# Performance work log

Hardware: AMD Instinct MI355X
Metric: run time of the kernel (lower is better)

## Reference

```python
import jax, jax.numpy as jnp
import numpy as np

N_NODES = 40000
N_EDGES = 640000
EMBED = 128
L = 3
EPS = 1e-5


def bn(x, g, b):
    # BatchNorm1d in training mode: batch mean / biased variance over axis 0
    m = jnp.mean(x, axis=0)
    v = jnp.var(x, axis=0)
    return (x - m) * jax.lax.rsqrt(v + EPS) * g + b


def setup_inputs() -> dict:
    key = jax.random.key(0)
    ks = jax.random.split(key, 16)
    d = {}
    d["node_attr"] = jax.random.normal(ks[0], (N_NODES, 2), jnp.float32)
    d["edge_index"] = jax.random.randint(ks[1], (2, N_EDGES), 0, N_NODES, jnp.int32)
    d["edge_attr"] = jax.random.normal(ks[2], (N_EDGES, 1), jnp.float32)
    s = 0.1
    d["W0"] = jax.random.normal(ks[3], (2, EMBED), jnp.float32) * s
    d["b0"] = jnp.zeros((EMBED,), jnp.float32)
    d["g0"] = jnp.ones((EMBED,), jnp.float32)
    d["bt0"] = jnp.zeros((EMBED,), jnp.float32)
    d["Wnode"] = jax.random.normal(ks[4], (L, EMBED, EMBED), jnp.float32) * s
    d["bnode"] = jnp.zeros((L, EMBED), jnp.float32)
    d["Wedge"] = jax.random.normal(ks[5], (L, 1, EMBED), jnp.float32) * s
    d["bedge"] = jnp.zeros((L, EMBED), jnp.float32)
    d["Wnb"] = jax.random.normal(ks[6], (L, EMBED, EMBED), jnp.float32) * s
    d["bnb"] = jnp.zeros((L, EMBED), jnp.float32)
    for nm in ("gn", "ge", "gnb", "gm1", "gm2"):
        d[nm] = jnp.ones((L, EMBED), jnp.float32)
    for nm in ("btn", "bte", "btnb", "btm1", "btm2"):
        d[nm] = jnp.zeros((L, EMBED), jnp.float32)
    d["Wm1"] = jax.random.normal(ks[7], (L, EMBED, EMBED), jnp.float32) * s
    d["bm1"] = jnp.zeros((L, EMBED), jnp.float32)
    d["Wm2"] = jax.random.normal(ks[8], (L, EMBED, EMBED), jnp.float32) * s
    d["bm2"] = jnp.zeros((L, EMBED), jnp.float32)
    return d


def reference(node_attr, edge_index, edge_attr,
              W0, b0, g0, bt0,
              Wnode, bnode, Wedge, bedge, Wnb, bnb,
              gn, btn, ge, bte, gnb, btnb,
              Wm1, bm1, gm1, btm1, Wm2, bm2, gm2, btm2):
    row, col = edge_index[0], edge_index[1]
    n = node_attr.shape[0]
    # initial node MLP (applied once, before layer 0)
    x = jax.nn.relu(bn(node_attr @ W0 + b0, g0, bt0))  # [N, E]
    for i in range(L):
        # edge branch: linear on raw edge_attr, scatter-add to source nodes (row)
        ea = edge_attr @ Wedge[i] + bedge[i]                      # [Ne, E]
        ea = jax.ops.segment_sum(ea, row, num_segments=n)         # [N, E]
        ea = bn(ea, ge[i], bte[i])
        # neighbor branch: h_j gathered from sources, aggregated at targets (col)
        h = x @ Wnb[i] + bnb[i]                                   # [N, E]
        aggr = jax.ops.segment_sum(h[row], col, num_segments=n)   # [N, E]
        # node branch
        xn = bn(x @ Wnode[i] + bnode[i], gn[i], btn[i])
        # update MLP
        y = jax.nn.relu(xn + bn(aggr, gnb[i], btnb[i]) + ea)
        y = jax.nn.relu(bn(y @ Wm1[i] + bm1[i], gm1[i], btm1[i]))
        y = jax.nn.relu(bn(y @ Wm2[i] + bm2[i], gm2[i], btm2[i]))
        x = y
    return x
```

## Files before the change

kernel.cpp:

```cpp
#include <hip/hip_runtime.h>

#define N_NODES 40000
#define N_EDGES 640000
#define EMB 128
#define NF ((size_t)N_NODES * EMB)
#define RCP_N (1.0f / (float)N_NODES)
#define BN_EPS 1e-5f
#define CAP 64
#define NSLICE 16
#define STB (NSLICE * 256)
#define GB 625

typedef _Float16 f16x8v __attribute__((ext_vector_type(8)));
typedef float f32x4v __attribute__((ext_vector_type(4)));
typedef unsigned short ushort8v __attribute__((ext_vector_type(8)));

__device__ __forceinline__ unsigned short f2h(float v) {
    return __builtin_bit_cast(unsigned short, (_Float16)v);
}
__device__ __forceinline__ float h2f(unsigned short u) {
    return (float)__builtin_bit_cast(_Float16, u);
}

__device__ __forceinline__ void bn_prep(
    const float* __restrict__ stat, const float* __restrict__ g,
    const float* __restrict__ bt, float* C, float* D, int t)
{
    if (t < 128) {
        float sm = 0.f, sq = 0.f;
        #pragma unroll
        for (int s = 0; s < NSLICE; ++s) {
            sm += stat[s * 256 + t];
            sq += stat[s * 256 + 128 + t];
        }
        float m = sm * RCP_N;
        float v = sq * RCP_N - m * m;
        float a = g[t] * rsqrtf(v + BN_EPS);
        C[t] = a; D[t] = bt[t] - m * a;
    }
}

__global__ __launch_bounds__(256) void edge_init_kernel(
    const float* __restrict__ na, const float* __restrict__ W0,
    const float* __restrict__ b0, unsigned short* __restrict__ Z,
    float* __restrict__ st,
    const int* __restrict__ ei, const float* __restrict__ ea,
    unsigned long long* __restrict__ scP, unsigned* __restrict__ cursor,
    int* __restrict__ slot)
{
    __shared__ float red[256];
    const int blk = blockIdx.x;
    const int t = threadIdx.x;
    if (blk < 625) {
        int col = t & 127, rh = t >> 7;
        float w0 = W0[col], w1 = W0[128 + col], bb = b0[col];
        int rbase = blk * 64;
        float sm = 0.f, sq = 0.f;
        #pragma unroll 4
        for (int i = 0; i < 32; ++i) {
            int r = rbase + rh + i * 2;
            float2 nv = *(const float2*)&na[r * 2];
            float v = fmaf(nv.x, w0, fmaf(nv.y, w1, bb));
            Z[(size_t)r * 128 + col] = f2h(v);
            sm += v; sq += v * v;
        }
        float* stS = st + (blk & (NSLICE - 1)) * 256;
        red[t] = sm; __syncthreads();
        if (t < 128) atomicAdd(&stS[t], red[t] + red[t + 128]);
        __syncthreads();
        red[t] = sq; __syncthreads();
        if (t < 128) atomicAdd(&stS[128 + t], red[t] + red[t + 128]);
    } else {
        int e = (blk - 625) * 256 + t;
        int r = ei[e];
        int d = ei[N_EDGES + e];
        int fx = (int)rintf(ea[e] * 65536.0f);
        unsigned long long add =
            (((unsigned long long)(unsigned)(fx + 0x40000000)) << 20) | 1ULL;
        atomicAdd(&scP[r], add);
        unsigned pos = atomicAdd(&cursor[d], 1u);
        slot[(size_t)d * CAP + (pos < CAP ? pos : CAP - 1)] = r;
    }
}

__global__ __launch_bounds__(256) void decode_kernel(
    const unsigned long long* __restrict__ scP, const unsigned* __restrict__ cursor,
    float* __restrict__ sN, float* __restrict__ cN, float* __restrict__ dgf,
    float* __restrict__ mom)
{
    int t = threadIdx.x;
    int i = blockIdx.x * 256 + t;
    float a0 = 0.f, a1 = 0.f, a2 = 0.f, a3 = 0.f, a4 = 0.f;
    if (i < N_NODES) {
        unsigned long long v = scP[i];
        unsigned cnt = (unsigned)(v & 0xFFFFFULL);
        long long sp = (long long)(v >> 20) - ((long long)cnt << 30);
        float s = (float)sp * (1.0f / 65536.0f);
        float c = (float)cnt;
        sN[i] = s; cN[i] = c;
        dgf[i] = (float)cursor[i];
        a0 = s; a1 = s * s; a2 = c; a3 = c * c; a4 = s * c;
    }
    #pragma unroll
    for (int off = 32; off > 0; off >>= 1) {
        a0 += __shfl_down(a0, off);
        a1 += __shfl_down(a1, off);
        a2 += __shfl_down(a2, off);
        a3 += __shfl_down(a3, off);
        a4 += __shfl_down(a4, off);
    }
    if ((t & 63) == 0) {
        atomicAdd(&mom[0], a0);
        atomicAdd(&mom[1], a1);
        atomicAdd(&mom[2], a2);
        atomicAdd(&mom[3], a3);
        atomicAdd(&mom[4], a4);
    }
}

__global__ __launch_bounds__(256) void wprep_kernel(
    const float* __restrict__ Wnode, const float* __restrict__ Wnb,
    const float* __restrict__ Wm1, const float* __restrict__ Wm2,
    unsigned short* __restrict__ Wt)
{
    __shared__ float tile[32][129];
    int b = blockIdx.x;
    int mat = b >> 2, kc = (b & 3) * 32;
    int grp = mat / 3, lay = mat % 3;
    const float* src = (grp == 0) ? Wnode : (grp == 1) ? Wnb : (grp == 2) ? Wm1 : Wm2;
    src += (size_t)lay * 16384;
    int t = threadIdx.x;
    #pragma unroll
    for (int i = 0; i < 16; ++i) {
        int idx = t + i * 256;
        int r = idx >> 7, n = idx & 127;
        tile[r][n] = src[(size_t)(kc + r) * 128 + n];
    }
    __syncthreads();
    int n = t >> 1, h = (t & 1) * 16;
    ushort8v o0, o1;
    #pragma unroll
    for (int j = 0; j < 8; ++j) o0[j] = f2h(tile[h + j][n]);
    #pragma unroll
    for (int j = 0; j < 8; ++j) o1[j] = f2h(tile[h + 8 + j][n]);
    unsigned short* dst = &Wt[(size_t)mat * 16384 + n * 128 + kc + h];
    *(ushort8v*)dst = o0;
    *(ushort8v*)(dst + 8) = o1;
}

__global__ __launch_bounds__(256) void gather_bn_kernel(
    const unsigned* __restrict__ cnt, const int* __restrict__ slot,
    const unsigned short* __restrict__ Ph,
    const float* __restrict__ stat, const float* __restrict__ g_in,
    const float* __restrict__ bt_in,
    unsigned short* __restrict__ Gh)
{
    __shared__ float aT[128], bT[128];
    int t = threadIdx.x;
    bn_prep(stat, g_in, bt_in, aT, bT, t);
    __syncthreads();
    int wid = (blockIdx.x * 256 + t) >> 6;
    int lane = t & 63;
    int q = lane >> 4, l16 = lane & 15;
    int cb = l16 * 8;
    float av[8], bv[8];
    #pragma unroll
    for (int k = 0; k < 8; ++k) { av[k] = aT[cb + k]; bv[k] = bT[cb + k]; }
    int n = (int)cnt[wid];
    n = n < CAP ? n : CAP;
    const int* sl = &slot[(size_t)wid * CAP];
    float s0[8] = {0}, s1[8] = {0};
    int j = q;
    for (; j + 4 < n; j += 8) {
        int r0 = sl[j], r1 = sl[j + 4];
        ushort8v v0 = *(const ushort8v*)&Ph[(size_t)r0 * 128 + cb];
        ushort8v v1 = *(const ushort8v*)&Ph[(size_t)r1 * 128 + cb];
        #pragma unroll
        for (int k = 0; k < 8; ++k) {
            s0[k] += fmaxf(0.f, fmaf(h2f(v0[k]), av[k], bv[k]));
            s1[k] += fmaxf(0.f, fmaf(h2f(v1[k]), av[k], bv[k]));
        }
    }
    for (; j < n; j += 4) {
        int r0 = sl[j];
        ushort8v v0 = *(const ushort8v*)&Ph[(size_t)r0 * 128 + cb];
        #pragma unroll
        for (int k = 0; k < 8; ++k)
            s0[k] += fmaxf(0.f, fmaf(h2f(v0[k]), av[k], bv[k]));
    }
    #pragma unroll
    for (int k = 0; k < 8; ++k) {
        float v = s0[k] + s1[k];
        v += __shfl_xor(v, 16);
        v += __shfl_xor(v, 32);
        s0[k] = v;
    }
    if (q == 0) {
        ushort8v o;
        #pragma unroll
        for (int k = 0; k < 8; ++k) o[k] = f2h(s0[k]);
        *(ushort8v*)&Gh[(size_t)wid * 128 + cb] = o;
    }
}

template<int AMODE, bool RSC>
__device__ __forceinline__ void gemm_body(
    int row0, int t, int slice,
    const unsigned short* __restrict__ A, const unsigned short* __restrict__ A2,
    const unsigned short* __restrict__ Wt,
    const float* __restrict__ bias, const float* __restrict__ rowscale,
    const float* C1, const float* D1, const float* C2, const float* D2,
    const float* AE, const float* BE, const float* CE,
    const float* __restrict__ sN, const float* __restrict__ cN,
    unsigned short* __restrict__ Out, float* __restrict__ stats_out,
    unsigned short* Bs, float (*redS)[128], float (*redQ)[128])
{
    #pragma unroll
    for (int i = 0; i < 8; ++i) {
        int cch = t + i * 256;
        int n = cch >> 4, off = (cch & 15) << 3;
        ushort8v w = *(const ushort8v*)&Wt[n * 128 + off];
        *(ushort8v*)&Bs[(n * 128 + off) ^ ((n & 7) << 3)] = w;
    }

    const int w = t >> 6, lane = t & 63;
    const int la = lane & 15, lb = lane >> 4;
    const int ar = row0 + (w << 4) + la;
    const int kb = lb * 8;

    f16x8v afrag[4];
    #pragma unroll
    for (int s = 0; s < 4; ++s) {
        ushort8v avv = *(const ushort8v*)&A[(size_t)ar * 128 + s * 32 + kb];
        if (AMODE == 0) {
            afrag[s] = __builtin_bit_cast(f16x8v, avv);
        } else if (AMODE == 1) {
            f16x8v o;
            #pragma unroll
            for (int j = 0; j < 8; ++j) {
                int qq = s * 32 + kb + j;
                o[j] = (_Float16)fmaxf(0.f, fmaf(h2f(avv[j]), C1[qq], D1[qq]));
            }
            afrag[s] = o;
        } else {
            ushort8v gv = *(const ushort8v*)&A2[(size_t)ar * 128 + s * 32 + kb];
            float sr = sN[ar], cr = cN[ar];
            f16x8v o;
            #pragma unroll
            for (int j = 0; j < 8; ++j) {
                int qq = s * 32 + kb + j;
                float y = h2f(avv[j]) * C1[qq] + D1[qq] + h2f(gv[j]) * C2[qq] + D2[qq]
                        + sr * AE[qq] + cr * BE[qq] + CE[qq];
                o[j] = (_Float16)fmaxf(0.f, y);
            }
            afrag[s] = o;
        }
    }
    __syncthreads();

    f32x4v acc[8];
    #pragma unroll
    for (int c = 0; c < 8; ++c) acc[c] = (f32x4v){0.f, 0.f, 0.f, 0.f};

    #pragma unroll
    for (int c = 0; c < 8; ++c) {
        int bn_ = (c << 4) + la;
        int bbase = bn_ * 128;
        int bswz = (bn_ & 7) << 3;
        #pragma unroll
        for (int s = 0; s < 4; ++s) {
            f16x8v bf = *(const f16x8v*)&Bs[(bbase + s * 32 + kb) ^ bswz];
            acc[c] = __builtin_amdgcn_mfma_f32_16x16x32_f16(
                afrag[s], bf, acc[c], 0, 0, 0);
        }
    }

    const int orow0 = row0 + (w << 4) + lb * 4;
    float rsj[4];
    if (RSC) {
        #pragma unroll
        for (int j = 0; j < 4; ++j) rsj[j] = rowscale[orow0 + j];
    }
    float csum[8], csq[8];
    #pragma unroll
    for (int c = 0; c < 8; ++c) {
        int col = (c << 4) + la;
        float bc = bias[col];
        float s0 = 0.f, s1 = 0.f;
        #pragma unroll
        for (int j = 0; j < 4; ++j) {
            float v = acc[c][j] + (RSC ? rsj[j] * bc : bc);
            Out[(size_t)(orow0 + j) * 128 + col] = f2h(v);
            s0 += v; s1 += v * v;
        }
        csum[c] = s0; csq[c] = s1;
    }
    #pragma unroll
    for (int c = 0; c < 8; ++c) {
        csum[c] += __shfl_xor(csum[c], 16);
        csum[c] += __shfl_xor(csum[c], 32);
        csq[c]  += __shfl_xor(csq[c], 16);
        csq[c]  += __shfl_xor(csq[c], 32);
    }
    if (lane < 16) {
        #pragma unroll
        for (int c = 0; c < 8; ++c) {
            redS[w][(c << 4) + lane] = csum[c];
            redQ[w][(c << 4) + lane] = csq[c];
        }
    }
    __syncthreads();
    float* stS = stats_out + slice * 256;
    if (t < 128) {
        atomicAdd(&stS[t], redS[0][t] + redS[1][t] + redS[2][t] + redS[3][t]);
        atomicAdd(&stS[128 + t], redQ[0][t] + redQ[1][t] + redQ[2][t] + redQ[3][t]);
    }
}

__global__ __launch_bounds__(256) void dual_gemm_kernel(
    const unsigned short* __restrict__ Ph, unsigned short* __restrict__ Gh,
    const unsigned short* __restrict__ WtZ, const unsigned short* __restrict__ WtG,
    const float* __restrict__ bZ, const float* __restrict__ bG,
    const float* __restrict__ dg,
    const float* __restrict__ st1, const float* __restrict__ g1,
    const float* __restrict__ bt1,
    unsigned short* __restrict__ ZNh,
    float* __restrict__ statZN, float* __restrict__ statG)
{
    __shared__ __align__(16) unsigned short Bs[128 * 128];
    __shared__ float C1[128], D1[128];
    __shared__ float redS[4][128], redQ[4][128];
    const int t = threadIdx.x;
    const int b = blockIdx.x;

    if (b < GB) {
        bn_prep(st1, g1, bt1, C1, D1, t);
        __syncthreads();
        gemm_body<1, false>(b * 64, t, b & (NSLICE - 1),
            Ph, nullptr, WtZ, bZ, nullptr,
            C1, D1, nullptr, nullptr, nullptr, nullptr, nullptr,
            nullptr, nullptr, ZNh, statZN, Bs, redS, redQ);
    } else {
        gemm_body<0, true>((b - GB) * 64, t, b & (NSLICE - 1),
            Gh, nullptr, WtG, bG, dg,
            nullptr, nullptr, nullptr, nullptr, nullptr, nullptr, nullptr,
            nullptr, nullptr, Gh, statG, Bs, redS, redQ);
    }
}

template<int AMODE, bool RSC>
__global__ __launch_bounds__(256) void mfma_gemm_kernel(
    const unsigned short* __restrict__ A, const unsigned short* __restrict__ A2,
    const unsigned short* __restrict__ Wt,
    const float* __restrict__ bias, const float* __restrict__ rowscale,
    const float* __restrict__ st1, const float* __restrict__ g1, const float* __restrict__ bt1,
    const float* __restrict__ st2, const float* __restrict__ g2, const float* __restrict__ bt2,
    const float* __restrict__ sN, const float* __restrict__ cN,
    const float* __restrict__ scal,
    const float* __restrict__ We, const float* __restrict__ Be,
    const float* __restrict__ ge, const float* __restrict__ bte,
    unsigned short* __restrict__ Out, float* __restrict__ stats_out)
{
    __shared__ __align__(16) unsigned short Bs[128 * 128];
    __shared__ float C1[128], D1[128], C2[128], D2[128];
    __shared__ float AE[128], BE[128], CE[128];
    __shared__ float redS[4][128], redQ[4][128];
    const int t = threadIdx.x;

    if (AMODE >= 1) {
        bn_prep(st1, g1, bt1, C1, D1, t);
    }
    if (AMODE == 2) {
        bn_prep(st2, g2, bt2, C2, D2, t);
        if (t < 128) {
            float ms = scal[0] * RCP_N, vs = scal[1] * RCP_N - ms * ms;
            float mc = scal[2] * RCP_N, vc = scal[3] * RCP_N - mc * mc;
            float cov = scal[4] * RCP_N - ms * mc;
            float we = We[t], be = Be[t];
            float me = ms * we + mc * be;
            float ve = we * we * vs + be * be * vc + 2.f * we * be * cov;
            float ae = ge[t] * rsqrtf(ve + BN_EPS);
            AE[t] = we * ae; BE[t] = be * ae; CE[t] = bte[t] - me * ae;
        }
    }
    if (AMODE >= 1) __syncthreads();

    gemm_body<AMODE, RSC>(blockIdx.x * 64, t, blockIdx.x & (NSLICE - 1),
        A, A2, Wt, bias, rowscale,
        C1, D1, C2, D2, AE, BE, CE,
        sN, cN, Out, stats_out, Bs, redS, redQ);
}

__global__ __launch_bounds__(256) void bnrelu_kernel(
    const unsigned short* __restrict__ Z, const float* __restrict__ stz,
    const float* __restrict__ g, const float* __restrict__ bt,
    float* __restrict__ O)
{
    __shared__ float aT[128], bT[128];
    int t = threadIdx.x;
    bn_prep(stz, g, bt, aT, bT, t);
    __syncthreads();
    int stride = gridDim.x * 256;
    for (int idx = blockIdx.x * 256 + t; idx < N_NODES * 32; idx += stride) {
        int r = idx >> 5;
        int q = (idx & 31) * 4;
        ushort4 z = *(const ushort4*)&Z[(size_t)r * 128 + q];
        float4 o;
        o.x = fmaxf(0.f, fmaf(h2f(z.x), aT[q],     bT[q]));
        o.y = fmaxf(0.f, fmaf(h2f(z.y), aT[q + 1], bT[q + 1]));
        o.z = fmaxf(0.f, fmaf(h2f(z.z), aT[q + 2], bT[q + 2]));
        o.w = fmaxf(0.f, fmaf(h2f(z.w), aT[q + 3], bT[q + 3]));
        *(float4*)&O[(size_t)r * 128 + q] = o;
    }
}

extern "C" void kernel_launch(void* const* d_in, const int* in_sizes, int n_in,
                              void* d_out, int out_size, void* d_ws, size_t ws_size,
                              hipStream_t stream)
{
    const float* node_attr = (const float*)d_in[0];
    const int*   ei        = (const int*)d_in[1];
    const float* ea        = (const float*)d_in[2];
    const float* W0    = (const float*)d_in[3];
    const float* b0    = (const float*)d_in[4];
    const float* g0    = (const float*)d_in[5];
    const float* bt0   = (const float*)d_in[6];
    const float* Wnode = (const float*)d_in[7];
    const float* bnode = (const float*)d_in[8];
    const float* Wedge = (const float*)d_in[9];
    const float* bedge = (const float*)d_in[10];
    const float* Wnb   = (const float*)d_in[11];
    const float* bnb   = (const float*)d_in[12];
    const float* gn    = (const float*)d_in[13];
    const float* ge    = (const float*)d_in[14];
    const float* gnb   = (const float*)d_in[15];
    const float* gm1   = (const float*)d_in[16];
    const float* gm2   = (const float*)d_in[17];
    const float* btn   = (const float*)d_in[18];
    const float* bte   = (const float*)d_in[19];
    const float* btnb  = (const float*)d_in[20];
    const float* btm1  = (const float*)d_in[21];
    const float* btm2  = (const float*)d_in[22];
    const float* Wm1   = (const float*)d_in[23];
    const float* bm1   = (const float*)d_in[24];
    const float* Wm2   = (const float*)d_in[25];
    const float* bm2   = (const float*)d_in[26];
    float* out = (float*)d_out;

    unsigned short* Ph  = (unsigned short*)d_ws;
    unsigned short* ZNh = Ph + NF;
    unsigned short* Gh  = ZNh + NF;
    float* sN = (float*)(Gh + NF);
    float* cN = sN + N_NODES;
    float* dg = cN + N_NODES;
    float* st = dg + N_NODES;
    const size_t ST_FLOATS = 256 + (size_t)STB * 13;
    unsigned long long* scP = (unsigned long long*)(st + ST_FLOATS);
    unsigned* cursor = (unsigned*)(scP + N_NODES);
    int* slot = (int*)(cursor + N_NODES);
    unsigned short* Wtb = (unsigned short*)(slot + (size_t)N_NODES * CAP);
    float* stInit = st + 256;
    float* layBase = st + 256 + STB;

    (void)hipMemsetAsync(st, 0, (ST_FLOATS + 3 * (size_t)N_NODES) * sizeof(float), stream);
    wprep_kernel<<<48, 256, 0, stream>>>(Wnode, Wnb, Wm1, Wm2, Wtb);
    edge_init_kernel<<<3125, 256, 0, stream>>>(
        node_attr, W0, b0, Ph, stInit, ei, ea, scP, cursor, slot);
    decode_kernel<<<157, 256, 0, stream>>>(scP, cursor, sN, cN, dg, st);

    const float* xst = stInit;
    const float* xg  = g0;
    const float* xbt = bt0;

    for (int i = 0; i < 3; ++i) {
        float* lay = layBase + (size_t)i * 4 * STB;
        gather_bn_kernel<<<10000, 256, 0, stream>>>(cursor, slot, Ph, xst, xg, xbt, Gh);
        dual_gemm_kernel<<<2 * GB, 256, 0, stream>>>(
            Ph, Gh,
            Wtb + (size_t)(0 + i) * 16384, Wtb + (size_t)(3 + i) * 16384,
            bnode + i * 128, bnb + i * 128, dg,
            xst, xg, xbt,
            ZNh, lay, lay + STB);
        mfma_gemm_kernel<2, false><<<GB, 256, 0, stream>>>(
            ZNh, Gh, Wtb + (size_t)(6 + i) * 16384, bm1 + i * 128, nullptr,
            lay, gn + i * 128, btn + i * 128,
            lay + STB, gnb + i * 128, btnb + i * 128,
            sN, cN, st,
            Wedge + i * 128, bedge + i * 128, ge + i * 128, bte + i * 128,
            ZNh, lay + 2 * STB);
        mfma_gemm_kernel<1, false><<<GB, 256, 0, stream>>>(
            ZNh, nullptr, Wtb + (size_t)(9 + i) * 16384, bm2 + i * 128, nullptr,
            lay + 2 * STB, gm1 + i * 128, btm1 + i * 128, nullptr, nullptr, nullptr,
            nullptr, nullptr, nullptr, nullptr, nullptr, nullptr, nullptr,
            Ph, lay + 3 * STB);

        xst = lay + 3 * STB;
        xg  = gm2 + i * 128;
        xbt = btm2 + i * 128;
    }
    bnrelu_kernel<<<2048, 256, 0, stream>>>(Ph, xst, xg, xbt, out);
}
```

Measured before the change: 309.4 us.

## Fuse neighbor gather-aggregation into dual GEMM kernel via shared-memory A tile

```diff
diff --git a/kernel.cpp b/kernel.cpp
--- a/kernel.cpp
+++ b/kernel.cpp
@@ -148,72 +148,78 @@
     *(ushort8v*)(dst + 8) = o1;
 }
 
-__global__ __launch_bounds__(256) void gather_bn_kernel(
-    const unsigned* __restrict__ cnt, const int* __restrict__ slot,
-    const unsigned short* __restrict__ Ph,
-    const float* __restrict__ stat, const float* __restrict__ g_in,
-    const float* __restrict__ bt_in,
-    unsigned short* __restrict__ Gh)
-{
-    __shared__ float aT[128], bT[128];
-    int t = threadIdx.x;
-    bn_prep(stat, g_in, bt_in, aT, bT, t);
+template<bool RSC>
+__device__ __forceinline__ void gemm_core(
+    int row0, int t, int slice, f16x8v afrag[4],
+    const float* __restrict__ bias, const float* __restrict__ rowscale,
+    unsigned short* __restrict__ Out, float* __restrict__ stats_out,
+    const unsigned short* Bs, float (*redS)[128], float (*redQ)[128])
+{
+    const int w = t >> 6, lane = t & 63;
+    const int la = lane & 15, lb = lane >> 4;
+    const int kb = lb * 8;
+
+    f32x4v acc[8];
+    #pragma unroll
+    for (int c = 0; c < 8; ++c) acc[c] = (f32x4v){0.f, 0.f, 0.f, 0.f};
+
+    #pragma unroll
+    for (int c = 0; c < 8; ++c) {
+        int bn_ = (c << 4) + la;
+        int bbase = bn_ * 128;
+        int bswz = (bn_ & 7) << 3;
+        #pragma unroll
+        for (int s = 0; s < 4; ++s) {
+            f16x8v bf = *(const f16x8v*)&Bs[(bbase + s * 32 + kb) ^ bswz];
+            acc[c] = __builtin_amdgcn_mfma_f32_16x16x32_f16(
+                afrag[s], bf, acc[c], 0, 0, 0);
+        }
+    }
+
+    const int orow0 = row0 + (w << 4) + lb * 4;
+    float rsj[4];
+    if (RSC) {
+        #pragma unroll
+        for (int j = 0; j < 4; ++j) rsj[j] = rowscale[orow0 + j];
+    }
+    float csum[8], csq[8];
+    #pragma unroll
+    for (int c = 0; c < 8; ++c) {
+        int col = (c << 4) + la;
+        float bc = bias[col];
+        float s0 = 0.f, s1 = 0.f;
+        #pragma unroll
+        for (int j = 0; j < 4; ++j) {
+            float v = acc[c][j] + (RSC ? rsj[j] * bc : bc);
+            Out[(size_t)(orow0 + j) * 128 + col] = f2h(v);
+            s0 += v; s1 += v * v;
+        }
+        csum[c] = s0; csq[c] = s1;
+    }
+    #pragma unroll
+    for (int c = 0; c < 8; ++c) {
+        csum[c] += __shfl_xor(csum[c], 16);
+        csum[c] += __shfl_xor(csum[c], 32);
+        csq[c]  += __shfl_xor(csq[c], 16);
+        csq[c]  += __shfl_xor(csq[c], 32);
+    }
+    if (lane < 16) {
+        #pragma unroll
+        for (int c = 0; c < 8; ++c) {
+            redS[w][(c << 4) + lane] = csum[c];
+            redQ[w][(c << 4) + lane] = csq[c];
+        }
+    }
     __syncthreads();
-    int wid = (blockIdx.x * 256 + t) >> 6;
-    int lane = t & 63;
-    int q = lane >> 4, l16 = lane & 15;
-    int cb = l16 * 8;
-    float av[8], bv[8];
-    #pragma unroll
-    for (int k = 0; k < 8; ++k) { av[k] = aT[cb + k]; bv[k] = bT[cb + k]; }
-    int n = (int)cnt[wid];
-    n = n < CAP ? n : CAP;
-    const int* sl = &slot[(size_t)wid * CAP];
-    float s0[8] = {0}, s1[8] = {0};
-    int j = q;
-    for (; j + 4 < n; j += 8) {
-        int r0 = sl[j], r1 = sl[j + 4];
-        ushort8v v0 = *(const ushort8v*)&Ph[(size_t)r0 * 128 + cb];
-        ushort8v v1 = *(const ushort8v*)&Ph[(size_t)r1 * 128 + cb];
-        #pragma unroll
-        for (int k = 0; k < 8; ++k) {
-            s0[k] += fmaxf(0.f, fmaf(h2f(v0[k]), av[k], bv[k]));
-            s1[k] += fmaxf(0.f, fmaf(h2f(v1[k]), av[k], bv[k]));
-        }
-    }
-    for (; j < n; j += 4) {
-        int r0 = sl[j];
-        ushort8v v0 = *(const ushort8v*)&Ph[(size_t)r0 * 128 + cb];
-        #pragma unroll
-        for (int k = 0; k < 8; ++k)
-            s0[k] += fmaxf(0.f, fmaf(h2f(v0[k]), av[k], bv[k]));
-    }
-    #pragma unroll
-    for (int k = 0; k < 8; ++k) {
-        float v = s0[k] + s1[k];
-        v += __shfl_xor(v, 16);
-        v += __shfl_xor(v, 32);
-        s0[k] = v;
-    }
-    if (q == 0) {
-        ushort8v o;
-        #pragma unroll
-        for (int k = 0; k < 8; ++k) o[k] = f2h(s0[k]);
-        *(ushort8v*)&Gh[(size_t)wid * 128 + cb] = o;
-    }
-}
-
-template<int AMODE, bool RSC>
-__device__ __forceinline__ void gemm_body(
-    int row0, int t, int slice,
-    const unsigned short* __restrict__ A, const unsigned short* __restrict__ A2,
-    const unsigned short* __restrict__ Wt,
-    const float* __restrict__ bias, const float* __restrict__ rowscale,
-    const float* C1, const float* D1, const float* C2, const float* D2,
-    const float* AE, const float* BE, const float* CE,
-    const float* __restrict__ sN, const float* __restrict__ cN,
-    unsigned short* __restrict__ Out, float* __restrict__ stats_out,
-    unsigned short* Bs, float (*redS)[128], float (*redQ)[128])
+    float* stS = stats_out + slice * 256;
+    if (t < 128) {
+        atomicAdd(&stS[t], redS[0][t] + redS[1][t] + redS[2][t] + redS[3][t]);
+        atomicAdd(&stS[128 + t], redQ[0][t] + redQ[1][t] + redQ[2][t] + redQ[3][t]);
+    }
+}
+
+__device__ __forceinline__ void stage_B(
+    const unsigned short* __restrict__ Wt, unsigned short* Bs, int t)
 {
     #pragma unroll
     for (int i = 0; i < 8; ++i) {
@@ -222,13 +228,20 @@
         ushort8v w = *(const ushort8v*)&Wt[n * 128 + off];
         *(ushort8v*)&Bs[(n * 128 + off) ^ ((n & 7) << 3)] = w;
     }
-
+}
+
+template<int AMODE>
+__device__ __forceinline__ void load_afrag_global(
+    int row0, int t, f16x8v afrag[4],
+    const unsigned short* __restrict__ A, const unsigned short* __restrict__ A2,
+    const float* C1, const float* D1, const float* C2, const float* D2,
+    const float* AE, const float* BE, const float* CE,
+    const float* __restrict__ sN, const float* __restrict__ cN)
+{
     const int w = t >> 6, lane = t & 63;
     const int la = lane & 15, lb = lane >> 4;
     const int ar = row0 + (w << 4) + la;
     const int kb = lb * 8;
-
-    f16x8v afrag[4];
     #pragma unroll
     for (int s = 0; s < 4; ++s) {
         ushort8v avv = *(const ushort8v*)&A[(size_t)ar * 128 + s * 32 + kb];
@@ -256,95 +269,89 @@
             afrag[s] = o;
         }
     }
-    __syncthreads();
-
-    f32x4v acc[8];
-    #pragma unroll
-    for (int c = 0; c < 8; ++c) acc[c] = (f32x4v){0.f, 0.f, 0.f, 0.f};
-
-    #pragma unroll
-    for (int c = 0; c < 8; ++c) {
-        int bn_ = (c << 4) + la;
-        int bbase = bn_ * 128;
-        int bswz = (bn_ & 7) << 3;
-        #pragma unroll
-        for (int s = 0; s < 4; ++s) {
-            f16x8v bf = *(const f16x8v*)&Bs[(bbase + s * 32 + kb) ^ bswz];
-            acc[c] = __builtin_amdgcn_mfma_f32_16x16x32_f16(
-                afrag[s], bf, acc[c], 0, 0, 0);
-        }
-    }
-
-    const int orow0 = row0 + (w << 4) + lb * 4;
-    float rsj[4];
-    if (RSC) {
-        #pragma unroll
-        for (int j = 0; j < 4; ++j) rsj[j] = rowscale[orow0 + j];
-    }
-    float csum[8], csq[8];
-    #pragma unroll
-    for (int c = 0; c < 8; ++c) {
-        int col = (c << 4) + la;
-        float bc = bias[col];
-        float s0 = 0.f, s1 = 0.f;
-        #pragma unroll
-        for (int j = 0; j < 4; ++j) {
-            float v = acc[c][j] + (RSC ? rsj[j] * bc : bc);
-            Out[(size_t)(orow0 + j) * 128 + col] = f2h(v);
-            s0 += v; s1 += v * v;
-        }
-        csum[c] = s0; csq[c] = s1;
-    }
-    #pragma unroll
-    for (int c = 0; c < 8; ++c) {
-        csum[c] += __shfl_xor(csum[c], 16);
-        csum[c] += __shfl_xor(csum[c], 32);
-        csq[c]  += __shfl_xor(csq[c], 16);
-        csq[c]  += __shfl_xor(csq[c], 32);
-    }
-    if (lane < 16) {
-        #pragma unroll
-        for (int c = 0; c < 8; ++c) {
-            redS[w][(c << 4) + lane] = csum[c];
-            redQ[w][(c << 4) + lane] = csq[c];
-        }
-    }
-    __syncthreads();
-    float* stS = stats_out + slice * 256;
-    if (t < 128) {
-        atomicAdd(&stS[t], redS[0][t] + redS[1][t] + redS[2][t] + redS[3][t]);
-        atomicAdd(&stS[128 + t], redQ[0][t] + redQ[1][t] + redQ[2][t] + redQ[3][t]);
-    }
 }
 
 __global__ __launch_bounds__(256) void dual_gemm_kernel(
-    const unsigned short* __restrict__ Ph, unsigned short* __restrict__ Gh,
+    const unsigned* __restrict__ cnt, const int* __restrict__ slot,
+    const unsigned short* __restrict__ Ph,
     const unsigned short* __restrict__ WtZ, const unsigned short* __restrict__ WtG,
     const float* __restrict__ bZ, const float* __restrict__ bG,
     const float* __restrict__ dg,
     const float* __restrict__ st1, const float* __restrict__ g1,
     const float* __restrict__ bt1,
-    unsigned short* __restrict__ ZNh,
+    unsigned short* __restrict__ ZNh, unsigned short* __restrict__ Gh,
     float* __restrict__ statZN, float* __restrict__ statG)
 {
     __shared__ __align__(16) unsigned short Bs[128 * 128];
+    __shared__ __align__(16) unsigned short As[64 * 128];
     __shared__ float C1[128], D1[128];
     __shared__ float redS[4][128], redQ[4][128];
     const int t = threadIdx.x;
     const int b = blockIdx.x;
 
+    bn_prep(st1, g1, bt1, C1, D1, t);
+    __syncthreads();
+
     if (b < GB) {
-        bn_prep(st1, g1, bt1, C1, D1, t);
+        const int row0 = b * 64;
+        stage_B(WtZ, Bs, t);
+        f16x8v afrag[4];
+        load_afrag_global<1>(row0, t, afrag, Ph, nullptr,
+                             C1, D1, nullptr, nullptr, nullptr, nullptr, nullptr,
+                             nullptr, nullptr);
         __syncthreads();
-        gemm_body<1, false>(b * 64, t, b & (NSLICE - 1),
-            Ph, nullptr, WtZ, bZ, nullptr,
-            C1, D1, nullptr, nullptr, nullptr, nullptr, nullptr,
-            nullptr, nullptr, ZNh, statZN, Bs, redS, redQ);
+        gemm_core<false>(row0, t, b & (NSLICE - 1), afrag, bZ, nullptr,
+                         ZNh, statZN, Bs, redS, redQ);
     } else {
-        gemm_body<0, true>((b - GB) * 64, t, b & (NSLICE - 1),
-            Gh, nullptr, WtG, bG, dg,
-            nullptr, nullptr, nullptr, nullptr, nullptr, nullptr, nullptr,
-            nullptr, nullptr, Gh, statG, Bs, redS, redQ);
+        const int row0 = (b - GB) * 64;
+        stage_B(WtG, Bs, t);
+        const int w = t >> 6, lane = t & 63;
+        const int q = lane >> 4, l16 = lane & 15;
+        const int cb = l16 * 8;
+        float av[8], bv[8];
+        #pragma unroll
+        for (int k = 0; k < 8; ++k) { av[k] = C1[cb + k]; bv[k] = D1[cb + k]; }
+        #pragma unroll
+        for (int i = 0; i < 4; ++i) {
+            int nl = (w << 4) + i * 4 + q;
+            int node = row0 + nl;
+            int n = (int)cnt[node];
+            n = n < CAP ? n : CAP;
+            const int* sl = &slot[(size_t)node * CAP];
+            float s0[8] = {0}, s1[8] = {0};
+            int j = 0;
+            for (; j + 1 < n; j += 2) {
+                int r0 = sl[j], r1 = sl[j + 1];
+                ushort8v v0 = *(const ushort8v*)&Ph[(size_t)r0 * 128 + cb];
+                ushort8v v1 = *(const ushort8v*)&Ph[(size_t)r1 * 128 + cb];
+                #pragma unroll
+                for (int k = 0; k < 8; ++k) {
+                    s0[k] += fmaxf(0.f, fmaf(h2f(v0[k]), av[k], bv[k]));
+                    s1[k] += fmaxf(0.f, fmaf(h2f(v1[k]), av[k], bv[k]));
+                }
+            }
+            if (j < n) {
+                ushort8v v0 = *(const ushort8v*)&Ph[(size_t)sl[j] * 128 + cb];
+                #pragma unroll
+                for (int k = 0; k < 8; ++k)
+                    s0[k] += fmaxf(0.f, fmaf(h2f(v0[k]), av[k], bv[k]));
+            }
+            ushort8v o;
+            #pragma unroll
+            for (int k = 0; k < 8; ++k) o[k] = f2h(s0[k] + s1[k]);
+            *(ushort8v*)&As[(nl * 128 + cb) ^ ((nl & 7) << 3)] = o;
+        }
+        __syncthreads();
+        const int la = lane & 15, lb = lane >> 4;
+        const int arl = (w << 4) + la;
+        const int abase = arl * 128 + lb * 8;
+        const int aswz = (arl & 7) << 3;
+        f16x8v afrag[4];
+        #pragma unroll
+        for (int s = 0; s < 4; ++s)
+            afrag[s] = *(const f16x8v*)&As[(abase + (s << 5)) ^ aswz];
+        gemm_core<true>(row0, t, b & (NSLICE - 1), afrag, bG, dg,
+                        Gh, statG, Bs, redS, redQ);
     }
 }
 
@@ -385,10 +392,14 @@
     }
     if (AMODE >= 1) __syncthreads();
 
-    gemm_body<AMODE, RSC>(blockIdx.x * 64, t, blockIdx.x & (NSLICE - 1),
-        A, A2, Wt, bias, rowscale,
-        C1, D1, C2, D2, AE, BE, CE,
-        sN, cN, Out, stats_out, Bs, redS, redQ);
+    const int row0 = blockIdx.x * 64;
+    stage_B(Wt, Bs, t);
+    f16x8v afrag[4];
+    load_afrag_global<AMODE>(row0, t, afrag, A, A2,
+                             C1, D1, C2, D2, AE, BE, CE, sN, cN);
+    __syncthreads();
+    gemm_core<RSC>(row0, t, blockIdx.x & (NSLICE - 1), afrag, bias, rowscale,
+                   Out, stats_out, Bs, redS, redQ);
 }
 
 __global__ __launch_bounds__(256) void bnrelu_kernel(
@@ -474,13 +485,12 @@
 
     for (int i = 0; i < 3; ++i) {
         float* lay = layBase + (size_t)i * 4 * STB;
-        gather_bn_kernel<<<10000, 256, 0, stream>>>(cursor, slot, Ph, xst, xg, xbt, Gh);
         dual_gemm_kernel<<<2 * GB, 256, 0, stream>>>(
-            Ph, Gh,
+            cursor, slot, Ph,
             Wtb + (size_t)(0 + i) * 16384, Wtb + (size_t)(3 + i) * 16384,
             bnode + i * 128, bnb + i * 128, dg,
             xst, xg, xbt,
-            ZNh, lay, lay + STB);
+            ZNh, Gh, lay, lay + STB);
         mfma_gemm_kernel<2, false><<<GB, 256, 0, stream>>>(
             ZNh, Gh, Wtb + (size_t)(6 + i) * 16384, bm1 + i * 128, nullptr,
             lay, gn + i * 128, btn + i * 128,
```

New measurement: 434.5 us. +40.4%, slower.
